# Kernel tuning notes

Hardware: AMD Instinct MI355X
Metric: run time of the kernel (lower is better)

## Reference

```python
import jax, jax.numpy as jnp
import numpy as np

B, CIN, T = 32, 16, 4096
H, DEPTH, E, K = 192, 4, 4, 7
DILATIONS = (1, 2, 4, 8)
NUM_BANDS, P = 16, 8
HM = 2 * H  # mlp_ratio = 2.0
NCLS = 50
GAIN_LIMIT = 0.5
EPS = 1e-5


def _rbf_basis(num_bins, num_bands):
    freqs = jnp.linspace(0.0, 1.0, num_bins)
    centers = jnp.linspace(0.0, 1.0, num_bands)
    width = 1.5 / (num_bands - 1)
    basis = jnp.exp(-0.5 * ((freqs[None, :] - centers[:, None]) / width) ** 2)
    return basis / jnp.clip(basis.sum(-1, keepdims=True), 1e-8)


def _layernorm(x, g, b):
    m = x.mean(-1, keepdims=True)
    v = x.var(-1, keepdims=True)
    return (x - m) / jnp.sqrt(v + EPS) * g + b


def _groupnorm1(x, g, b):
    # GroupNorm(1, C): normalize over (C, T) per sample, per-channel affine
    m = x.mean((1, 2), keepdims=True)
    v = x.var((1, 2), keepdims=True)
    return (x - m) / jnp.sqrt(v + EPS) * g[None, :, None] + b[None, :, None]


def _bn_eval(x, g, b):
    # eval-mode BatchNorm1d with running_mean=0, running_var=1
    return x * (g / jnp.sqrt(1.0 + EPS))[None, :, None] + b[None, :, None]


def _gelu(x):
    return jax.nn.gelu(x, approximate=False)


def _dwconv(x, w, dilation):
    pad = (K // 2) * dilation
    return jax.lax.conv_general_dilated(
        x, w, (1,), [(pad, pad)], rhs_dilation=(dilation,),
        dimension_numbers=("NCH", "OIH", "NCH"), feature_group_count=x.shape[1])


def setup_inputs() -> dict:
    key = jax.random.key(0)
    ks = jax.random.split(key, 12)
    return {
        "x": jax.random.normal(ks[0], (B, CIN, T), jnp.float32),
        "stem_w": jax.random.normal(ks[1], (H, CIN, 3)) * 0.1,
        "stem_bn_g": jnp.ones((H,)), "stem_bn_b": jnp.zeros((H,)),
        "ln_g": jnp.ones((NUM_BANDS,)), "ln_b": jnp.zeros((NUM_BANDS,)),
        "proj_w": jax.random.normal(ks[2], (NUM_BANDS, NUM_BANDS)) * 0.25,
        "prototypes": jax.random.normal(ks[3], (P, NUM_BANDS)) * 0.02,
        "route_lib": jax.random.normal(ks[4], (P, DEPTH, E)) * 0.1,
        "gain_lib": jax.random.normal(ks[5], (P, DEPTH, H)) * 0.1,
        "norm1_g": jnp.ones((DEPTH, H)), "norm1_b": jnp.zeros((DEPTH, H)),
        "expert_w": jax.random.normal(ks[6], (DEPTH, E, H, 1, K)) * 0.2,
        "mix_w": jax.random.normal(ks[7], (DEPTH, H, H)) * (1.0 / np.sqrt(H)),
        "mix_bn_g": jnp.ones((DEPTH, H)), "mix_bn_b": jnp.zeros((DEPTH, H)),
        "norm2_g": jnp.ones((DEPTH, H)), "norm2_b": jnp.zeros((DEPTH, H)),
        "mlp_w1": jax.random.normal(ks[8], (DEPTH, HM, H)) * (1.0 / np.sqrt(H)),
        "mlp_b1": jnp.zeros((DEPTH, HM)),
        "mlp_w2": jax.random.normal(ks[9], (DEPTH, H, HM)) * (1.0 / np.sqrt(HM)),
        "mlp_b2": jnp.zeros((DEPTH, H)),
        "head_w": jax.random.normal(ks[10], (NCLS, H)) * (1.0 / np.sqrt(H)),
        "head_b": jnp.zeros((NCLS,)),
    }


def reference(x, stem_w, stem_bn_g, stem_bn_b, ln_g, ln_b, proj_w, prototypes,
              route_lib, gain_lib, norm1_g, norm1_b, expert_w, mix_w, mix_bn_g,
              mix_bn_b, norm2_g, norm2_b, mlp_w1, mlp_b1, mlp_w2, mlp_b2,
              head_w, head_b):
    # --- SpectralSummary ---
    spec = jnp.fft.rfft(x.astype(jnp.float32), axis=-1, norm="ortho")
    mag = jnp.abs(spec).mean(axis=1)                      # [B, bins]
    basis = _rbf_basis(mag.shape[-1], NUM_BANDS)          # [bands, bins]
    summary = jnp.log1p(mag) @ basis.T                    # [B, bands]
    # --- PrototypeRouter ---
    s = _layernorm(summary, ln_g, ln_b)
    rs = s @ proj_w.T
    logits = -((rs[:, None, :] - prototypes[None]) ** 2).mean(-1)  # [B, P]
    assign = jax.nn.softmax(logits * np.sqrt(NUM_BANDS), axis=-1)
    routes = jax.nn.softmax(jnp.einsum("bp,pde->bde", assign, route_lib), axis=-1)  # [B,D,E]
    gains = 1.0 + GAIN_LIMIT * jnp.tanh(jnp.einsum("bp,pdc->bdc", assign, gain_lib))  # [B,D,C]
    # --- Backbone stem ---
    z = jax.lax.conv_general_dilated(x, stem_w, (1,), [(1, 1)],
                                     dimension_numbers=("NCH", "OIH", "NCH"))
    z = _gelu(_bn_eval(z, stem_bn_g, stem_bn_b))
    # --- Routed temporal blocks ---
    for d in range(DEPTH):
        zn = _groupnorm1(z, norm1_g[d], norm1_b[d])
        pieces = jnp.stack([_dwconv(zn, expert_w[d, e], DILATIONS[e]) for e in range(E)], axis=1)  # [B,E,C,T]
        mixed = jnp.einsum("be,bect->bct", routes[:, d], pieces)
        mixed = mixed * gains[:, d][:, :, None]
        mixed = _gelu(_bn_eval(jnp.einsum("oc,bct->bot", mix_w[d], mixed), mix_bn_g[d], mix_bn_b[d]))
        z = z + mixed
        zn2 = _groupnorm1(z, norm2_g[d], norm2_b[d])
        h = _gelu(jnp.einsum("oc,bct->bot", mlp_w1[d], zn2) + mlp_b1[d][None, :, None])
        z = z + jnp.einsum("oc,bct->bot", mlp_w2[d], h) + mlp_b2[d][None, :, None]
    # --- Head: global average pool + linear ---
    pooled = z.mean(-1)
    return pooled @ head_w.T + head_b
```

## Files before the change

### kernel.cpp

```cpp
#include <hip/hip_runtime.h>
#include <math.h>

constexpr int cB = 32, cCIN = 16, cT = 4096, cH = 192, cD = 4, cE = 4, cK = 7;
constexpr int cBANDS = 16, cP = 8, cHM = 384, cNCLS = 50, cBINS = 2049;
constexpr float cEPS = 1e-5f;
constexpr int TT = 64, HALO = 24;
constexpr int ZSTR = 112;
constexpr int NTAP = 19;
constexpr float INV_SQRT2 = 0.7071067811865475f;

typedef __bf16 bf16_t;
typedef bf16_t bf16x8 __attribute__((ext_vector_type(8)));
typedef float f32x4 __attribute__((ext_vector_type(4)));

constexpr int OFFS[NTAP] = {-24,-16,-12,-8,-6,-4,-3,-2,-1,0,1,2,3,4,6,8,12,16,24};
constexpr int IDXT[cE][cK] = {
    {6, 7, 8, 9, 10, 11, 12},
    {4, 5, 7, 9, 11, 13, 14},
    {2, 3, 5, 9, 13, 15, 16},
    {0, 1, 3, 9, 15, 17, 18}};

__device__ __forceinline__ int xcd_swz(int bid) {
    return (bid & 7) * 256 + (bid >> 3);
}

__device__ __forceinline__ float fast_erf(float x) {
    float ax = fabsf(x);
    float t = 1.0f / fmaf(0.3275911f, ax, 1.0f);
    float p = t * fmaf(t, fmaf(t, fmaf(t, fmaf(t, 1.061405429f, -1.453152027f),
                                       1.421413741f), -0.284496736f), 0.254829592f);
    float e = __expf(-ax * ax);
    float r = 1.0f - p * e;
    return copysignf(r, x);
}
__device__ __forceinline__ float gelu_exact(float v) {
    return 0.5f * v * (1.0f + fast_erf(v * INV_SQRT2));
}
__device__ __forceinline__ unsigned short f2bf(float f) {
    union { float f; unsigned u; } v; v.f = f;
    unsigned r = (v.u + 0x7FFFu + ((v.u >> 16) & 1u)) >> 16;
    return (unsigned short)r;
}
__device__ __forceinline__ float bf2f(unsigned short u) {
    union { unsigned u; float f; } v; v.u = ((unsigned)u) << 16;
    return v.f;
}

__global__ __launch_bounds__(256) void k_zero(float* __restrict__ p, int n) {
    int i = blockIdx.x * 256 + threadIdx.x;
    if (i < n) p[i] = 0.f;
}

__global__ __launch_bounds__(256) void k_cvt(const float* __restrict__ src,
                                             unsigned short* __restrict__ dst, int n) {
    int i = blockIdx.x * 256 + threadIdx.x;
    if (i < n) dst[i] = f2bf(src[i]);
}

__global__ __launch_bounds__(256) void k_cvt_w2perm(const float* __restrict__ src,
                                                    unsigned short* __restrict__ dst, int n) {
    int j = blockIdx.x * 256 + threadIdx.x;
    if (j >= n) return;
    int dd = j / (cH * cHM);
    int rem = j % (cH * cHM);
    int o = rem / cHM, m = rem % cHM;
    int wid = m / 96;
    int rr = m % 96;
    int chunk = rr / 48;
    int ii = rr % 48;
    int pos = chunk * 192 + wid * 48 + ii;
    dst[(size_t)dd * cH * cHM + (size_t)o * cHM + pos] = f2bf(src[j]);
}

__global__ __launch_bounds__(256) void k_twiddle(float2* __restrict__ tw) {
    int ls = blockIdx.x;
    int n = cT >> ls;
    int cnt = n >> 1;
    int base = cT - (cT >> ls);
    for (int p = threadIdx.x; p < cnt; p += 256) {
        float ang = -6.283185307179586f * (float)p / (float)n;
        float sv, cv;
        sincosf(ang, &sv, &cv);
        tw[base + p] = make_float2(cv, sv);
    }
}

__global__ __launch_bounds__(256) void k_fft_mag(const float* __restrict__ x,
                                                 const float2* __restrict__ tw,
                                                 float* __restrict__ mag) {
    constexpr int N2 = cT / 2;
    __shared__ float Sr[2][N2];
    __shared__ float Si[2][N2];
    int b = blockIdx.x / cCIN, c = blockIdx.x % cCIN;
    const float* xp = x + ((size_t)b * cCIN + c) * cT;
#pragma unroll
    for (int it = 0; it < N2 / 256; it++) {
        int t = threadIdx.x + it * 256;
        float2 v = *reinterpret_cast<const float2*>(&xp[2 * t]);
        Sr[0][t] = v.x; Si[0][t] = v.y;
    }
    __syncthreads();
    int cur = 0;
    for (int ls = 0; ls < 11; ls++) {
        int s = 1 << ls;
        int twb = cT - (cT >> (ls + 1));
#pragma unroll
        for (int it = 0; it < N2 / 512; it++) {
            int j = threadIdx.x + it * 256;
            int p = j >> ls;
            float2 w = tw[twb + p];
            float wr = w.x, wi = w.y;
            int ia = j, ib = j + N2 / 2;
            float ar = Sr[cur][ia], ai = Si[cur][ia];
            float br = Sr[cur][ib], bi = Si[cur][ib];
            int oa = j + (j & ~(s - 1));
            int ob = oa + s;
            Sr[cur ^ 1][oa] = ar + br;
            Si[cur ^ 1][oa] = ai + bi;
            float tr = ar - br, ti = ai - bi;
            Sr[cur ^ 1][ob] = tr * wr - ti * wi;
            Si[cur ^ 1][ob] = tr * wi + ti * wr;
        }
        __syncthreads();
        cur ^= 1;
    }
    const float scale = (1.0f / 64.0f) * (1.0f / 16.0f);
    for (int k = threadIdx.x; k <= N2; k += 256) {
        int k2 = k & (N2 - 1), km = (N2 - k) & (N2 - 1);
        float yr = Sr[cur][k2], yi = Si[cur][k2];
        float zr = Sr[cur][km], zi = Si[cur][km];
        float Ar = 0.5f * (yr + zr), Ai = 0.5f * (yi - zi);
        float Br = 0.5f * (yi + zi), Bi = -0.5f * (yr - zr);
        float wr, wi;
        if (k < N2) { float2 w = tw[k]; wr = w.x; wi = w.y; }
        else { wr = -1.f; wi = 0.f; }
        float Xr = Ar + wr * Br - wi * Bi;
        float Xi = Ai + wr * Bi + wi * Br;
        atomicAdd(&mag[b * cBINS + k], sqrtf(Xr * Xr + Xi * Xi) * scale);
    }
}

__global__ __launch_bounds__(256) void k_basis(float* __restrict__ basis) {
    __shared__ float vals[cBINS];
    __shared__ float red[256];
    int band = blockIdx.x;
    float cb = (float)band / 15.0f;
    float inv_w = 15.0f / 1.5f;
    float local = 0.f;
    for (int k = threadIdx.x; k < cBINS; k += 256) {
        float f = (float)k / 2048.0f;
        float u = (f - cb) * inv_w;
        float v = expf(-0.5f * u * u);
        vals[k] = v;
        local += v;
    }
    red[threadIdx.x] = local;
    __syncthreads();
    for (int s = 128; s > 0; s >>= 1) {
        if (threadIdx.x < s) red[threadIdx.x] += red[threadIdx.x + s];
        __syncthreads();
    }
    float inv_sum = 1.0f / fmaxf(red[0], 1e-8f);
    for (int k = threadIdx.x; k < cBINS; k += 256)
        basis[band * cBINS + k] = vals[k] * inv_sum;
}

__global__ __launch_bounds__(256) void k_summary(const float* __restrict__ mag,
                                                 const float* __restrict__ basis,
                                                 float* __restrict__ summary) {
    int b = blockIdx.x;
    float acc[cBANDS];
#pragma unroll
    for (int i = 0; i < cBANDS; i++) acc[i] = 0.f;
    for (int k = threadIdx.x; k < cBINS; k += 256) {
        float lm = log1pf(mag[b * cBINS + k]);
#pragma unroll
        for (int band = 0; band < cBANDS; band++) acc[band] += lm * basis[band * cBINS + k];
    }
    __shared__ float red[cBANDS][256];
#pragma unroll
    for (int band = 0; band < cBANDS; band++) red[band][threadIdx.x] = acc[band];
    __syncthreads();
    for (int s = 128; s > 0; s >>= 1) {
        if (threadIdx.x < s)
#pragma unroll
            for (int band = 0; band < cBANDS; band++)
                red[band][threadIdx.x] += red[band][threadIdx.x + s];
        __syncthreads();
    }
    if (threadIdx.x < cBANDS) summary[b * cBANDS + threadIdx.x] = red[threadIdx.x][0];
}

__global__ __launch_bounds__(64) void k_router(
    const float* __restrict__ summary, const float* __restrict__ ln_g,
    const float* __restrict__ ln_b, const float* __restrict__ proj_w,
    const float* __restrict__ prototypes, const float* __restrict__ route_lib,
    const float* __restrict__ gain_lib, float* __restrict__ routes,
    float* __restrict__ gains) {
    int b = threadIdx.x;
    if (b >= cB) return;
    float s[cBANDS];
    float mean = 0.f;
#pragma unroll
    for (int i = 0; i < cBANDS; i++) { s[i] = summary[b * cBANDS + i]; mean += s[i]; }
    mean *= (1.0f / cBANDS);
    float var = 0.f;
#pragma unroll
    for (int i = 0; i < cBANDS; i++) { float d = s[i] - mean; var += d * d; }
    var *= (1.0f / cBANDS);
    float rstd = rsqrtf(var + cEPS);
#pragma unroll
    for (int i = 0; i < cBANDS; i++) s[i] = (s[i] - mean) * rstd * ln_g[i] + ln_b[i];
    float rs[cBANDS];
#pragma unroll
    for (int j = 0; j < cBANDS; j++) {
        float a = 0.f;
#pragma unroll
        for (int i = 0; i < cBANDS; i++) a += s[i] * proj_w[j * cBANDS + i];
        rs[j] = a;
    }
    float logits[cP];
    float mx = -1e30f;
#pragma unroll
    for (int p = 0; p < cP; p++) {
        float a = 0.f;
#pragma unroll
        for (int j = 0; j < cBANDS; j++) {
            float d = rs[j] - prototypes[p * cBANDS + j];
            a += d * d;
        }
        logits[p] = -(a * (1.0f / cBANDS)) * 4.0f;
        mx = fmaxf(mx, logits[p]);
    }
    float assign[cP];
    float denom = 0.f;
#pragma unroll
    for (int p = 0; p < cP; p++) { assign[p] = expf(logits[p] - mx); denom += assign[p]; }
    float invden = 1.0f / denom;
#pragma unroll
    for (int p = 0; p < cP; p++) assign[p] *= invden;
    for (int d = 0; d < cD; d++) {
        float r[cE];
        float rmx = -1e30f;
#pragma unroll
        for (int e = 0; e < cE; e++) {
            float a = 0.f;
#pragma unroll
            for (int p = 0; p < cP; p++) a += assign[p] * route_lib[(p * cD + d) * cE + e];
            r[e] = a;
            rmx = fmaxf(rmx, a);
        }
        float rden = 0.f;
#pragma unroll
        for (int e = 0; e < cE; e++) { r[e] = expf(r[e] - rmx); rden += r[e]; }
        float rinv = 1.0f / rden;
#pragma unroll
        for (int e = 0; e < cE; e++) routes[(b * cD + d) * cE + e] = r[e] * rinv;
        for (int c = 0; c < cH; c++) {
            float a = 0.f;
#pragma unroll
            for (int p = 0; p < cP; p++) a += assign[p] * gain_lib[(p * cD + d) * cH + c];
            gains[((size_t)b * cD + d) * cH + c] = 1.0f + 0.5f * tanhf(a);
        }
    }
}

__global__ __launch_bounds__(192) void k_weff(const float* __restrict__ ew_all,
                                              const float* __restrict__ routes,
                                              unsigned short* __restrict__ weff_g) {
    int bd = blockIdx.x;
    int d = bd % cD;
    int c = threadIdx.x;
    float rte[cE];
#pragma unroll
    for (int e = 0; e < cE; e++) rte[e] = routes[bd * cE + e];
    float acc[NTAP];
#pragma unroll
    for (int o = 0; o < NTAP; o++) acc[o] = 0.f;
#pragma unroll
    for (int e = 0; e < cE; e++) {
#pragma unroll
        for (int k = 0; k < cK; k++)
            acc[IDXT[e][k]] += rte[e] * ew_all[(((size_t)d * cE + e) * cH + c) * cK + k];
    }
    unsigned short* dst = weff_g + ((size_t)bd * cH + c) * 20;
#pragma unroll
    for (int o = 0; o < NTAP; o++) dst[o] = f2bf(acc[o]);
    dst[NTAP] = 0;
}

constexpr int STT = 256;
__global__ __launch_bounds__(256) void k_stem(const float* __restrict__ x,
                                              const float* __restrict__ stem_w,
                                              const float* __restrict__ bn_g,
                                              const float* __restrict__ bn_b,
                                              float* __restrict__ z,
                                              float* __restrict__ sums_out) {
    __shared__ float xs[cCIN][STT + 2];
    __shared__ float ws[cH * cCIN * 3];
    int blk = blockIdx.x;
    int b = blk / (cT / STT);
    int t0 = (blk % (cT / STT)) * STT;
    for (int i = threadIdx.x; i < cH * cCIN * 3; i += 256) ws[i] = stem_w[i];
    for (int i = threadIdx.x; i < cCIN * (STT + 2); i += 256) {
        int c = i / (STT + 2), tt = i % (STT + 2);
        int gt = t0 + tt - 1;
        xs[c][tt] = (gt >= 0 && gt < cT) ? x[((size_t)b * cCIN + c) * cT + gt] : 0.f;
    }
    __syncthreads();
    int tt = threadIdx.x;
    float xv[cCIN][3];
#pragma unroll
    for (int c = 0; c < cCIN; c++)
#pragma unroll
        for (int k = 0; k < 3; k++) xv[c][k] = xs[c][tt + k];
    int gt = t0 + tt;
    float bnrs = rsqrtf(1.0f + cEPS);
    float s = 0.f, q = 0.f;
    for (int h = 0; h < cH; h++) {
        const float* w = &ws[h * cCIN * 3];
        float acc = 0.f;
#pragma unroll
        for (int c = 0; c < cCIN; c++)
#pragma unroll
            for (int k = 0; k < 3; k++) acc += xv[c][k] * w[c * 3 + k];
        float v = acc * (bn_g[h] * bnrs) + bn_b[h];
        float res = gelu_exact(v);
        z[((size_t)b * cH + h) * cT + gt] = res;
        s += res; q += res * res;
    }
#pragma unroll
    for (int off = 32; off > 0; off >>= 1) { s += __shfl_down(s, off); q += __shfl_down(q, off); }
    if ((threadIdx.x & 63) == 0) {
        atomicAdd(&sums_out[b * 2], s);
        atomicAdd(&sums_out[b * 2 + 1], q);
    }
}

__global__ __launch_bounds__(256, 2) void k_block1(
    const float* __restrict__ zin, float* __restrict__ zout,
    const float* __restrict__ sums_in, float* __restrict__ sums_out,
    const float* __restrict__ g1, const float* __restrict__ b1,
    const unsigned short* __restrict__ weff_g, const unsigned short* __restrict__ mwb,
    const float* __restrict__ mg, const float* __restrict__ mb,
    const float* __restrict__ gains, int d) {
    __shared__ unsigned short zn[cH][ZSTR];
    __shared__ unsigned short mxT[TT][200];
    int blk = xcd_swz(blockIdx.x);
    int b = blk / (cT / TT);
    int t0 = (blk % (cT / TT)) * TT;
    int tid = threadIdx.x;
    const float invN = 1.0f / (float)(cH * cT);
    float mean = sums_in[b * 2] * invN;
    float var = sums_in[b * 2 + 1] * invN - mean * mean;
    float rstd = rsqrtf(var + cEPS);
    constexpr int S_ITERS = cH * 28 / 256;
    bool interior = (t0 >= HALO) && (t0 + TT + HALO <= cT);
    if (interior) {
#pragma unroll
        for (int it = 0; it < S_ITERS; it++) {
            int i = tid + it * 256;
            int c = i / 28, tt = (i % 28) * 4;
            int gt = t0 + tt - HALO;
            float gc = g1[c], bc = b1[c];
            float4 v = *reinterpret_cast<const float4*>(&zin[((size_t)b * cH + c) * cT + gt]);
            ushort4 pk;
            pk.x = f2bf((v.x - mean) * rstd * gc + bc);
            pk.y = f2bf((v.y - mean) * rstd * gc + bc);
            pk.z = f2bf((v.z - mean) * rstd * gc + bc);
            pk.w = f2bf((v.w - mean) * rstd * gc + bc);
            *reinterpret_cast<ushort4*>(&zn[c][tt]) = pk;
        }
    } else {
#pragma unroll
        for (int it = 0; it < S_ITERS; it++) {
            int i = tid + it * 256;
            int c = i / 28, tt = (i % 28) * 4;
            int gt = t0 + tt - HALO;
            float gc = g1[c], bc = b1[c];
            const float* zp = &zin[((size_t)b * cH + c) * cT];
            float n0 = (gt + 0 >= 0 && gt + 0 < cT) ? (zp[gt + 0] - mean) * rstd * gc + bc : 0.f;
            float n1 = (gt + 1 >= 0 && gt + 1 < cT) ? (zp[gt + 1] - mean) * rstd * gc + bc : 0.f;
            float n2 = (gt + 2 >= 0 && gt + 2 < cT) ? (zp[gt + 2] - mean) * rstd * gc + bc : 0.f;
            float n3 = (gt + 3 >= 0 && gt + 3 < cT) ? (zp[gt + 3] - mean) * rstd * gc + bc : 0.f;
            ushort4 pk;
            pk.x = f2bf(n0); pk.y = f2bf(n1); pk.z = f2bf(n2); pk.w = f2bf(n3);
            *reinterpret_cast<ushort4*>(&zn[c][tt]) = pk;
        }
    }
    int lane = tid & 63, wid = tid >> 6;
    int lrow = lane & 15;
    int lk8 = (lane >> 4) << 3;
    int r0 = (lane >> 4) << 2;
    int mbase = wid * 48;
    float res[3][4][4];
#pragma unroll
    for (int mt = 0; mt < 3; mt++)
#pragma unroll
        for (int nt = 0; nt < 4; nt++)
#pragma unroll
            for (int r = 0; r < 4; r++)
                res[mt][nt][r] = zin[((size_t)b * cH + mbase + mt * 16 + r0 + r) * cT +
                                     t0 + nt * 16 + lrow];
    __syncthreads();
    if (tid < cH) {
        int c = tid;
        const unsigned short* wp = weff_g + ((size_t)(b * cD + d) * cH + c) * 20;
        float wv[NTAP];
#pragma unroll
        for (int o = 0; o < NTAP; o++) wv[o] = bf2f(wp[o]);
        float g = gains[((size_t)b * cD + d) * cH + c];
        float win[ZSTR];
#pragma unroll
        for (int v = 0; v < 14; v++) {
            bf16x8 w8 = *reinterpret_cast<const bf16x8*>(&zn[c][8 * v]);
#pragma unroll
            for (int u = 0; u < 8; u++) win[8 * v + u] = (float)w8[u];
        }
#pragma unroll
        for (int t = 0; t < TT; t++) {
            float a = 0.f;
#pragma unroll
            for (int o = 0; o < NTAP; o++)
                a = fmaf(wv[o], win[t + HALO + OFFS[o]], a);
            mxT[t][c] = f2bf(a * g);
        }
    }
    __syncthreads();
    f32x4 acc[3][4];
#pragma unroll
    for (int mt = 0; mt < 3; mt++)
#pragma unroll
        for (int nt = 0; nt < 4; nt++)
#pragma unroll
            for (int r = 0; r < 4; r++) acc[mt][nt][r] = 0.f;
#pragma unroll
    for (int kk = 0; kk < 6; kk++) {
        int k0 = kk * 32 + lk8;
        bf16x8 a0 = *reinterpret_cast<const bf16x8*>(&mwb[(size_t)(mbase + lrow) * cH + k0]);
        bf16x8 a1 = *reinterpret_cast<const bf16x8*>(&mwb[(size_t)(mbase + 16 + lrow) * cH + k0]);
        bf16x8 a2 = *reinterpret_cast<const bf16x8*>(&mwb[(size_t)(mbase + 32 + lrow) * cH + k0]);
#pragma unroll
        for (int nt = 0; nt < 4; nt++) {
            bf16x8 bf = *reinterpret_cast<const bf16x8*>(&mxT[nt * 16 + lrow][k0]);
            acc[0][nt] = __builtin_amdgcn_mfma_f32_16x16x32_bf16(a0, bf, acc[0][nt], 0, 0, 0);
            acc[1][nt] = __builtin_amdgcn_mfma_f32_16x16x32_bf16(a1, bf, acc[1][nt], 0, 0, 0);
            acc[2][nt] = __builtin_amdgcn_mfma_f32_16x16x32_bf16(a2, bf, acc[2][nt], 0, 0, 0);
        }
    }
    float bnrs = rsqrtf(1.0f + cEPS);
    float s = 0.f, q = 0.f;
#pragma unroll
    for (int mt = 0; mt < 3; mt++) {
#pragma unroll
        for (int nt = 0; nt < 4; nt++) {
#pragma unroll
            for (int r = 0; r < 4; r++) {
                int o = mbase + mt * 16 + r0 + r;
                int t = t0 + nt * 16 + lrow;
                size_t idx = ((size_t)b * cH + o) * cT + t;
                float val = res[mt][nt][r] + gelu_exact(acc[mt][nt][r] * (mg[o] * bnrs) + mb[o]);
                zout[idx] = val;
                s += val; q += val * val;
            }
        }
    }
#pragma unroll
    for (int off = 32; off > 0; off >>= 1) { s += __shfl_down(s, off); q += __shfl_down(q, off); }
    if (lane == 0) {
        atomicAdd(&sums_out[b * 2], s);
        atomicAdd(&sums_out[b * 2 + 1], q);
    }
}

__global__ __launch_bounds__(256, 2) void k_block2(
    float* __restrict__ z, const float* __restrict__ sums_in,
    float* __restrict__ sums_out,
    const float* __restrict__ g2, const float* __restrict__ b2,
    const unsigned short* __restrict__ w1b, const float* __restrict__ bb1,
    const unsigned short* __restrict__ w2p, const float* __restrict__ bb2) {
    __shared__ unsigned short znT[TT][200];
    __shared__ unsigned short hT[TT][200];
    int blk = xcd_swz(blockIdx.x);
    int b = blk / (cT / TT);
    int t0 = (blk % (cT / TT)) * TT;
    const float invN = 1.0f / (float)(cH * cT);
    float mean = sums_in[b * 2] * invN;
    float var = sums_in[b * 2 + 1] * invN - mean * mean;
    float rstd = rsqrtf(var + cEPS);
    constexpr int S_ITERS = cH * (TT / 4) / 256;
#pragma unroll
    for (int it = 0; it < S_ITERS; it++) {
        int i = threadIdx.x + it * 256;
        int c = i >> 4, t4 = (i & 15) << 2;
        float4 v = *reinterpret_cast<const float4*>(&z[((size_t)b * cH + c) * cT + t0 + t4]);
        float gc = g2[c], bc = b2[c];
        znT[t4 + 0][c] = f2bf((v.x - mean) * rstd * gc + bc);
        znT[t4 + 1][c] = f2bf((v.y - mean) * rstd * gc + bc);
        znT[t4 + 2][c] = f2bf((v.z - mean) * rstd * gc + bc);
        znT[t4 + 3][c] = f2bf((v.w - mean) * rstd * gc + bc);
    }
    int lane = threadIdx.x & 63, wid = threadIdx.x >> 6;
    int lrow = lane & 15;
    int lk8 = (lane >> 4) << 3;
    int r0 = (lane >> 4) << 2;
    int obase = wid * 48;
    float res[3][4][4];
#pragma unroll
    for (int mt = 0; mt < 3; mt++)
#pragma unroll
        for (int nt = 0; nt < 4; nt++)
#pragma unroll
            for (int r = 0; r < 4; r++)
                res[mt][nt][r] = z[((size_t)b * cH + obase + mt * 16 + r0 + r) * cT +
                                   t0 + nt * 16 + lrow];
    __syncthreads();
    f32x4 acc2[3][4];
#pragma unroll
    for (int mt = 0; mt < 3; mt++) {
#pragma unroll
        for (int r = 0; r < 4; r++) {
            float bv = bb2[obase + mt * 16 + r0 + r];
            acc2[mt][0][r] = bv; acc2[mt][1][r] = bv; acc2[mt][2][r] = bv; acc2[mt][3][r] = bv;
        }
    }
#pragma unroll
    for (int chunk = 0; chunk < 2; chunk++) {
        int mbase = wid * 96 + chunk * 48;
        f32x4 acc1[3][4];
#pragma unroll
        for (int mt = 0; mt < 3; mt++) {
#pragma unroll
            for (int r = 0; r < 4; r++) {
                float bv = bb1[mbase + mt * 16 + r0 + r];
                acc1[mt][0][r] = bv; acc1[mt][1][r] = bv; acc1[mt][2][r] = bv; acc1[mt][3][r] = bv;
            }
        }
#pragma unroll
        for (int kk = 0; kk < 6; kk++) {
            int k0 = kk * 32 + lk8;
            bf16x8 a0 = *reinterpret_cast<const bf16x8*>(&w1b[(size_t)(mbase + lrow) * cH + k0]);
            bf16x8 a1 = *reinterpret_cast<const bf16x8*>(&w1b[(size_t)(mbase + 16 + lrow) * cH + k0]);
            bf16x8 a2 = *reinterpret_cast<const bf16x8*>(&w1b[(size_t)(mbase + 32 + lrow) * cH + k0]);
#pragma unroll
            for (int nt = 0; nt < 4; nt++) {
                bf16x8 bf = *reinterpret_cast<const bf16x8*>(&znT[nt * 16 + lrow][k0]);
                acc1[0][nt] = __builtin_amdgcn_mfma_f32_16x16x32_bf16(a0, bf, acc1[0][nt], 0, 0, 0);
                acc1[1][nt] = __builtin_amdgcn_mfma_f32_16x16x32_bf16(a1, bf, acc1[1][nt], 0, 0, 0);
                acc1[2][nt] = __builtin_amdgcn_mfma_f32_16x16x32_bf16(a2, bf, acc1[2][nt], 0, 0, 0);
            }
        }
#pragma unroll
        for (int mt = 0; mt < 3; mt++) {
            int o0 = wid * 48 + mt * 16 + r0;
#pragma unroll
            for (int nt = 0; nt < 4; nt++) {
                int t = nt * 16 + lrow;
                ushort4 pk;
                pk.x = f2bf(gelu_exact(acc1[mt][nt][0]));
                pk.y = f2bf(gelu_exact(acc1[mt][nt][1]));
                pk.z = f2bf(gelu_exact(acc1[mt][nt][2]));
                pk.w = f2bf(gelu_exact(acc1[mt][nt][3]));
                *reinterpret_cast<ushort4*>(&hT[t][o0]) = pk;
            }
        }
        __syncthreads();
#pragma unroll
        for (int kk = 0; kk < 6; kk++) {
            int kl = kk * 32 + lk8;
            int kg = chunk * 192 + kl;
            bf16x8 a0 = *reinterpret_cast<const bf16x8*>(&w2p[(size_t)(obase + lrow) * cHM + kg]);
            bf16x8 a1 = *reinterpret_cast<const bf16x8*>(&w2p[(size_t)(obase + 16 + lrow) * cHM + kg]);
            bf16x8 a2 = *reinterpret_cast<const bf16x8*>(&w2p[(size_t)(obase + 32 + lrow) * cHM + kg]);
#pragma unroll
            for (int nt = 0; nt < 4; nt++) {
                bf16x8 bf = *reinterpret_cast<const bf16x8*>(&hT[nt * 16 + lrow][kl]);
                acc2[0][nt] = __builtin_amdgcn_mfma_f32_16x16x32_bf16(a0, bf, acc2[0][nt], 0, 0, 0);
                acc2[1][nt] = __builtin_amdgcn_mfma_f32_16x16x32_bf16(a1, bf, acc2[1][nt], 0, 0, 0);
                acc2[2][nt] = __builtin_amdgcn_mfma_f32_16x16x32_bf16(a2, bf, acc2[2][nt], 0, 0, 0);
            }
        }
        if (chunk == 0) __syncthreads();
    }
    float s = 0.f, q = 0.f;
#pragma unroll
    for (int mt = 0; mt < 3; mt++) {
#pragma unroll
        for (int nt = 0; nt < 4; nt++) {
#pragma unroll
            for (int r = 0; r < 4; r++) {
                int o = obase + mt * 16 + r0 + r;
                int t = t0 + nt * 16 + lrow;
                size_t idx = ((size_t)b * cH + o) * cT + t;
                float val = res[mt][nt][r] + acc2[mt][nt][r];
                z[idx] = val;
                s += val; q += val * val;
            }
        }
    }
#pragma unroll
    for (int off = 32; off > 0; off >>= 1) { s += __shfl_down(s, off); q += __shfl_down(q, off); }
    if (lane == 0) {
        atomicAdd(&sums_out[b * 2], s);
        atomicAdd(&sums_out[b * 2 + 1], q);
    }
}

__global__ __launch_bounds__(256) void k_pool(const float* __restrict__ z,
                                              float* __restrict__ pooled) {
    int bh = blockIdx.x;
    const float* zp = z + (size_t)bh * cT;
    float s = 0.f;
#pragma unroll
    for (int it = 0; it < cT / 256; it++) s += zp[threadIdx.x + it * 256];
    __shared__ float red[256];
    red[threadIdx.x] = s;
    __syncthreads();
    for (int st = 128; st > 0; st >>= 1) {
        if (threadIdx.x < st) red[threadIdx.x] += red[threadIdx.x + st];
        __syncthreads();
    }
    if (threadIdx.x == 0) pooled[bh] = red[0] * (1.0f / cT);
}

__global__ __launch_bounds__(256) void k_head(const float* __restrict__ pooled,
                                              const float* __restrict__ hw,
                                              const float* __restrict__ hb,
                                              float* __restrict__ out) {
    int i = blockIdx.x * 256 + threadIdx.x;
    if (i >= cB * cNCLS) return;
    int b = i / cNCLS, n = i % cNCLS;
    float acc = hb[n];
    const float* pw = pooled + b * cH;
    const float* wr = hw + n * cH;
    for (int h = 0; h < cH; h++) acc += pw[h] * wr[h];
    out[i] = acc;
}

extern "C" void kernel_launch(void* const* d_in, const int* in_sizes, int n_in,
                              void* d_out, int out_size, void* d_ws, size_t ws_size,
                              hipStream_t stream) {
    const float* x          = (const float*)d_in[0];
    const float* stem_w     = (const float*)d_in[1];
    const float* stem_bn_g  = (const float*)d_in[2];
    const float* stem_bn_b  = (const float*)d_in[3];
    const float* ln_g       = (const float*)d_in[4];
    const float* ln_b       = (const float*)d_in[5];
    const float* proj_w     = (const float*)d_in[6];
    const float* prototypes = (const float*)d_in[7];
    const float* route_lib  = (const float*)d_in[8];
    const float* gain_lib   = (const float*)d_in[9];
    const float* norm1_g    = (const float*)d_in[10];
    const float* norm1_b    = (const float*)d_in[11];
    const float* expert_w   = (const float*)d_in[12];
    const float* mix_w      = (const float*)d_in[13];
    const float* mix_bn_g   = (const float*)d_in[14];
    const float* mix_bn_b   = (const float*)d_in[15];
    const float* norm2_g    = (const float*)d_in[16];
    const float* norm2_b    = (const float*)d_in[17];
    const float* mlp_w1     = (const float*)d_in[18];
    const float* mlp_b1     = (const float*)d_in[19];
    const float* mlp_w2     = (const float*)d_in[20];
    const float* mlp_b2     = (const float*)d_in[21];
    const float* head_w     = (const float*)d_in[22];
    const float* head_b     = (const float*)d_in[23];

    float* ws = (float*)d_ws;
    size_t off = 0;
    const size_t ZN = (size_t)cB * cH * cT;
    float* zA      = ws + off; off += ZN;
    float* zB      = ws + off; off += ZN;
    float* mag     = ws + off; off += (size_t)cB * cBINS;
    float* sums    = ws + off; off += 9 * cB * 2;
    float* basis   = ws + off; off += (size_t)cBANDS * cBINS;
    float* summary = ws + off; off += cB * cBANDS;
    float* routes  = ws + off; off += cB * cD * cE;
    float* gains   = ws + off; off += (size_t)cB * cD * cH;
    float* pooled  = ws + off; off += cB * cH;
    float2* tw     = (float2*)(ws + off); off += 2 * (cT - 1) + 2;
    unsigned short* mixb = (unsigned short*)(ws + off); off += (size_t)cD * cH * cH / 2;
    unsigned short* w1b  = (unsigned short*)(ws + off); off += (size_t)cD * cHM * cH / 2;
    unsigned short* w2b  = (unsigned short*)(ws + off); off += (size_t)cD * cH * cHM / 2;
    unsigned short* weff = (unsigned short*)(ws + off); off += (size_t)cB * cD * cH * 20 / 2;

    int nz = cB * cBINS + 9 * cB * 2;
    k_zero<<<(nz + 255) / 256, 256, 0, stream>>>(mag, nz);

    k_cvt<<<(cD * cH * cH + 255) / 256, 256, 0, stream>>>(mix_w, mixb, cD * cH * cH);
    k_cvt<<<(cD * cHM * cH + 255) / 256, 256, 0, stream>>>(mlp_w1, w1b, cD * cHM * cH);
    k_cvt_w2perm<<<(cD * cH * cHM + 255) / 256, 256, 0, stream>>>(mlp_w2, w2b, cD * cH * cHM);

    k_twiddle<<<12, 256, 0, stream>>>(tw);
    k_fft_mag<<<cB * cCIN, 256, 0, stream>>>(x, tw, mag);
    k_basis<<<cBANDS, 256, 0, stream>>>(basis);
    k_summary<<<cB, 256, 0, stream>>>(mag, basis, summary);
    k_router<<<1, 64, 0, stream>>>(summary, ln_g, ln_b, proj_w, prototypes,
                                   route_lib, gain_lib, routes, gains);
    k_weff<<<cB * cD, 192, 0, stream>>>(expert_w, routes, weff);

    k_stem<<<cB * (cT / STT), 256, 0, stream>>>(x, stem_w, stem_bn_g, stem_bn_b, zA,
                                                sums + 0 * cB * 2);

    float* zi = zA;
    float* zo = zB;
    for (int d = 0; d < cD; d++) {
        k_block1<<<cB * (cT / TT), 256, 0, stream>>>(
            zi, zo, sums + (size_t)(2 * d) * cB * 2, sums + (size_t)(2 * d + 1) * cB * 2,
            norm1_g + d * cH, norm1_b + d * cH,
            weff, mixb + (size_t)d * cH * cH,
            mix_bn_g + d * cH, mix_bn_b + d * cH, gains, d);
        k_block2<<<cB * (cT / TT), 256, 0, stream>>>(
            zo, sums + (size_t)(2 * d + 1) * cB * 2, sums + (size_t)(2 * d + 2) * cB * 2,
            norm2_g + d * cH, norm2_b + d * cH,
            w1b + (size_t)d * cHM * cH, mlp_b1 + d * cHM,
            w2b + (size_t)d * cH * cHM, mlp_b2 + d * cH);
        float* t = zi; zi = zo; zo = t;
    }

    k_pool<<<cB * cH, 256, 0, stream>>>(zi, pooled);
    k_head<<<(cB * cNCLS + 255) / 256, 256, 0, stream>>>(pooled, head_w, head_b,
                                                         (float*)d_out);
}
```

Before: 1.205 ms.

## Store residual stream activations in bf16 instead of fp32

The residual activation buffers z passed between the stem, block1, block2 and pool kernels are now stored as bf16, which halves global memory traffic for these large tensors. Every reader converts back to fp32. The per-sample sums used for group norm are accumulated from the rounded values, so the statistics match the stored data. The trade is extra rounding error on the residual stream across all depths, and the uncoalesced 2-byte scalar loads and stores in the residual read and write paths may cost efficiency.

Measured after the change: 1.160 ms. 1.04x faster.

```diff
diff --git a/kernel.cpp b/kernel.cpp
--- a/kernel.cpp
+++ b/kernel.cpp
@@ -43,6 +43,14 @@
 }
 __device__ __forceinline__ float bf2f(unsigned short u) {
     union { unsigned u; float f; } v; v.u = ((unsigned)u) << 16;
+    return v.f;
+}
+__device__ __forceinline__ float bflo(unsigned u) {
+    union { unsigned u; float f; } v; v.u = u << 16;
+    return v.f;
+}
+__device__ __forceinline__ float bfhi(unsigned u) {
+    union { unsigned u; float f; } v; v.u = u & 0xFFFF0000u;
     return v.f;
 }
 
@@ -294,7 +302,7 @@
                                               const float* __restrict__ stem_w,
                                               const float* __restrict__ bn_g,
                                               const float* __restrict__ bn_b,
-                                              float* __restrict__ z,
+                                              unsigned short* __restrict__ z,
                                               float* __restrict__ sums_out) {
     __shared__ float xs[cCIN][STT + 2];
     __shared__ float ws[cH * cCIN * 3];
@@ -325,8 +333,9 @@
 #pragma unroll
             for (int k = 0; k < 3; k++) acc += xv[c][k] * w[c * 3 + k];
         float v = acc * (bn_g[h] * bnrs) + bn_b[h];
-        float res = gelu_exact(v);
-        z[((size_t)b * cH + h) * cT + gt] = res;
+        unsigned short rb = f2bf(gelu_exact(v));
+        float res = bf2f(rb);
+        z[((size_t)b * cH + h) * cT + gt] = rb;
         s += res; q += res * res;
     }
 #pragma unroll
@@ -338,7 +347,7 @@
 }
 
 __global__ __launch_bounds__(256, 2) void k_block1(
-    const float* __restrict__ zin, float* __restrict__ zout,
+    const unsigned short* __restrict__ zin, unsigned short* __restrict__ zout,
     const float* __restrict__ sums_in, float* __restrict__ sums_out,
     const float* __restrict__ g1, const float* __restrict__ b1,
     const unsigned short* __restrict__ weff_g, const unsigned short* __restrict__ mwb,
@@ -363,12 +372,12 @@
             int c = i / 28, tt = (i % 28) * 4;
             int gt = t0 + tt - HALO;
             float gc = g1[c], bc = b1[c];
-            float4 v = *reinterpret_cast<const float4*>(&zin[((size_t)b * cH + c) * cT + gt]);
+            ushort4 v = *reinterpret_cast<const ushort4*>(&zin[((size_t)b * cH + c) * cT + gt]);
             ushort4 pk;
-            pk.x = f2bf((v.x - mean) * rstd * gc + bc);
-            pk.y = f2bf((v.y - mean) * rstd * gc + bc);
-            pk.z = f2bf((v.z - mean) * rstd * gc + bc);
-            pk.w = f2bf((v.w - mean) * rstd * gc + bc);
+            pk.x = f2bf((bf2f(v.x) - mean) * rstd * gc + bc);
+            pk.y = f2bf((bf2f(v.y) - mean) * rstd * gc + bc);
+            pk.z = f2bf((bf2f(v.z) - mean) * rstd * gc + bc);
+            pk.w = f2bf((bf2f(v.w) - mean) * rstd * gc + bc);
             *reinterpret_cast<ushort4*>(&zn[c][tt]) = pk;
         }
     } else {
@@ -378,11 +387,11 @@
             int c = i / 28, tt = (i % 28) * 4;
             int gt = t0 + tt - HALO;
             float gc = g1[c], bc = b1[c];
-            const float* zp = &zin[((size_t)b * cH + c) * cT];
-            float n0 = (gt + 0 >= 0 && gt + 0 < cT) ? (zp[gt + 0] - mean) * rstd * gc + bc : 0.f;
-            float n1 = (gt + 1 >= 0 && gt + 1 < cT) ? (zp[gt + 1] - mean) * rstd * gc + bc : 0.f;
-            float n2 = (gt + 2 >= 0 && gt + 2 < cT) ? (zp[gt + 2] - mean) * rstd * gc + bc : 0.f;
-            float n3 = (gt + 3 >= 0 && gt + 3 < cT) ? (zp[gt + 3] - mean) * rstd * gc + bc : 0.f;
+            const unsigned short* zp = &zin[((size_t)b * cH + c) * cT];
+            float n0 = (gt + 0 >= 0 && gt + 0 < cT) ? (bf2f(zp[gt + 0]) - mean) * rstd * gc + bc : 0.f;
+            float n1 = (gt + 1 >= 0 && gt + 1 < cT) ? (bf2f(zp[gt + 1]) - mean) * rstd * gc + bc : 0.f;
+            float n2 = (gt + 2 >= 0 && gt + 2 < cT) ? (bf2f(zp[gt + 2]) - mean) * rstd * gc + bc : 0.f;
+            float n3 = (gt + 3 >= 0 && gt + 3 < cT) ? (bf2f(zp[gt + 3]) - mean) * rstd * gc + bc : 0.f;
             ushort4 pk;
             pk.x = f2bf(n0); pk.y = f2bf(n1); pk.z = f2bf(n2); pk.w = f2bf(n3);
             *reinterpret_cast<ushort4*>(&zn[c][tt]) = pk;
@@ -400,8 +409,8 @@
         for (int nt = 0; nt < 4; nt++)
 #pragma unroll
             for (int r = 0; r < 4; r++)
-                res[mt][nt][r] = zin[((size_t)b * cH + mbase + mt * 16 + r0 + r) * cT +
-                                     t0 + nt * 16 + lrow];
+                res[mt][nt][r] = bf2f(zin[((size_t)b * cH + mbase + mt * 16 + r0 + r) * cT +
+                                         t0 + nt * 16 + lrow]);
     __syncthreads();
     if (tid < cH) {
         int c = tid;
@@ -459,8 +468,10 @@
                 int o = mbase + mt * 16 + r0 + r;
                 int t = t0 + nt * 16 + lrow;
                 size_t idx = ((size_t)b * cH + o) * cT + t;
-                float val = res[mt][nt][r] + gelu_exact(acc[mt][nt][r] * (mg[o] * bnrs) + mb[o]);
-                zout[idx] = val;
+                unsigned short vb = f2bf(res[mt][nt][r] +
+                                         gelu_exact(acc[mt][nt][r] * (mg[o] * bnrs) + mb[o]));
+                float val = bf2f(vb);
+                zout[idx] = vb;
                 s += val; q += val * val;
             }
         }
@@ -474,7 +485,7 @@
 }
 
 __global__ __launch_bounds__(256, 2) void k_block2(
-    float* __restrict__ z, const float* __restrict__ sums_in,
+    unsigned short* __restrict__ z, const float* __restrict__ sums_in,
     float* __restrict__ sums_out,
     const float* __restrict__ g2, const float* __restrict__ b2,
     const unsigned short* __restrict__ w1b, const float* __restrict__ bb1,
@@ -493,12 +504,12 @@
     for (int it = 0; it < S_ITERS; it++) {
         int i = threadIdx.x + it * 256;
         int c = i >> 4, t4 = (i & 15) << 2;
-        float4 v = *reinterpret_cast<const float4*>(&z[((size_t)b * cH + c) * cT + t0 + t4]);
+        ushort4 v = *reinterpret_cast<const ushort4*>(&z[((size_t)b * cH + c) * cT + t0 + t4]);
         float gc = g2[c], bc = b2[c];
-        znT[t4 + 0][c] = f2bf((v.x - mean) * rstd * gc + bc);
-        znT[t4 + 1][c] = f2bf((v.y - mean) * rstd * gc + bc);
-        znT[t4 + 2][c] = f2bf((v.z - mean) * rstd * gc + bc);
-        znT[t4 + 3][c] = f2bf((v.w - mean) * rstd * gc + bc);
+        znT[t4 + 0][c] = f2bf((bf2f(v.x) - mean) * rstd * gc + bc);
+        znT[t4 + 1][c] = f2bf((bf2f(v.y) - mean) * rstd * gc + bc);
+        znT[t4 + 2][c] = f2bf((bf2f(v.z) - mean) * rstd * gc + bc);
+        znT[t4 + 3][c] = f2bf((bf2f(v.w) - mean) * rstd * gc + bc);
     }
     int lane = threadIdx.x & 63, wid = threadIdx.x >> 6;
     int lrow = lane & 15;
@@ -512,8 +523,8 @@
         for (int nt = 0; nt < 4; nt++)
 #pragma unroll
             for (int r = 0; r < 4; r++)
-                res[mt][nt][r] = z[((size_t)b * cH + obase + mt * 16 + r0 + r) * cT +
-                                   t0 + nt * 16 + lrow];
+                res[mt][nt][r] = bf2f(z[((size_t)b * cH + obase + mt * 16 + r0 + r) * cT +
+                                        t0 + nt * 16 + lrow]);
     __syncthreads();
     f32x4 acc2[3][4];
 #pragma unroll
@@ -592,8 +603,9 @@
                 int o = obase + mt * 16 + r0 + r;
                 int t = t0 + nt * 16 + lrow;
                 size_t idx = ((size_t)b * cH + o) * cT + t;
-                float val = res[mt][nt][r] + acc2[mt][nt][r];
-                z[idx] = val;
+                unsigned short vb = f2bf(res[mt][nt][r] + acc2[mt][nt][r]);
+                float val = bf2f(vb);
+                z[idx] = vb;
                 s += val; q += val * val;
             }
         }
@@ -606,13 +618,17 @@
     }
 }
 
-__global__ __launch_bounds__(256) void k_pool(const float* __restrict__ z,
+__global__ __launch_bounds__(256) void k_pool(const unsigned short* __restrict__ z,
                                               float* __restrict__ pooled) {
     int bh = blockIdx.x;
-    const float* zp = z + (size_t)bh * cT;
+    const unsigned short* zp = z + (size_t)bh * cT;
     float s = 0.f;
 #pragma unroll
-    for (int it = 0; it < cT / 256; it++) s += zp[threadIdx.x + it * 256];
+    for (int it = 0; it < 2; it++) {
+        uint4 v = *reinterpret_cast<const uint4*>(&zp[(threadIdx.x + it * 256) * 8]);
+        s += bflo(v.x) + bfhi(v.x) + bflo(v.y) + bfhi(v.y) +
+             bflo(v.z) + bfhi(v.z) + bflo(v.w) + bfhi(v.w);
+    }
     __shared__ float red[256];
     red[threadIdx.x] = s;
     __syncthreads();
@@ -668,8 +684,8 @@
     float* ws = (float*)d_ws;
     size_t off = 0;
     const size_t ZN = (size_t)cB * cH * cT;
-    float* zA      = ws + off; off += ZN;
-    float* zB      = ws + off; off += ZN;
+    unsigned short* zA = (unsigned short*)(ws + off); off += ZN / 2;
+    unsigned short* zB = (unsigned short*)(ws + off); off += ZN / 2;
     float* mag     = ws + off; off += (size_t)cB * cBINS;
     float* sums    = ws + off; off += 9 * cB * 2;
     float* basis   = ws + off; off += (size_t)cBANDS * cBINS;
@@ -701,8 +717,8 @@
     k_stem<<<cB * (cT / STT), 256, 0, stream>>>(x, stem_w, stem_bn_g, stem_bn_b, zA,
                                                 sums + 0 * cB * 2);
 
-    float* zi = zA;
-    float* zo = zB;
+    unsigned short* zi = zA;
+    unsigned short* zo = zB;
     for (int d = 0; d < cD; d++) {
         k_block1<<<cB * (cT / TT), 256, 0, stream>>>(
             zi, zo, sums + (size_t)(2 * d) * cB * 2, sums + (size_t)(2 * d + 1) * cB * 2,
@@ -714,7 +730,7 @@
             norm2_g + d * cH, norm2_b + d * cH,
             w1b + (size_t)d * cHM * cH, mlp_b1 + d * cHM,
             w2b + (size_t)d * cH * cHM, mlp_b2 + d * cH);
-        float* t = zi; zi = zo; zo = t;
+        unsigned short* t = zi; zi = zo; zo = t;
     }
 
     k_pool<<<cB * cH, 256, 0, stream>>>(zi, pooled);
```
